# Performance work log

Measured on AMD Instinct MI355X. Metric: run time of the kernel, lower is better.

Reference implementation:

```python
import jax, jax.numpy as jnp
import numpy as np

B, S, E, H = 8, 1024, 512, 8
NEG = -1e10


def setup_inputs() -> dict:
    key = jax.random.key(0)
    ks = jax.random.split(key, 8)
    k = jax.random.normal(ks[0], (B, S, E), dtype=jnp.float32)
    v = jax.random.normal(ks[1], (B, S, E), dtype=jnp.float32)
    q = jax.random.normal(ks[2], (B, S, E), dtype=jnp.float32)
    # causal mask, broadcastable like torch masked_fill
    mask = jnp.tril(jnp.ones((S, S), dtype=jnp.int32))[None, None]
    sc = 1.0 / np.sqrt(E)
    Wk = jax.random.normal(ks[3], (H * E, E), dtype=jnp.float32) * sc
    Wq = jax.random.normal(ks[4], (H * E, E), dtype=jnp.float32) * sc
    Wv = jax.random.normal(ks[5], (H * E, E), dtype=jnp.float32) * sc
    Wo = jax.random.normal(ks[6], (E, H * E), dtype=jnp.float32) * (1.0 / np.sqrt(H * E))
    bo = jnp.zeros((E,), dtype=jnp.float32)
    return {"k": k, "v": v, "q": q, "mask": mask,
            "Wk": Wk, "Wq": Wq, "Wv": Wv, "Wo": Wo, "bo": bo}


def reference(k, v, q, mask, Wk, Wq, Wv, Wo, bo):
    b, q_len, e = q.shape
    k_len, v_len = k.shape[1], v.shape[1]
    h = Wk.shape[0] // e
    scale = jnp.sqrt(jnp.asarray(e // h, dtype=jnp.float32))
    # projections E -> H*E (torch Linear: x @ W.T)
    wk = (k @ Wk.T).reshape(b, h, k_len, e)   # raw reshape, matches torch .view
    wq = (q @ Wq.T).reshape(b, h, q_len, e)
    wv = (v @ Wv.T).reshape(b, h, v_len, e)
    energy = jnp.einsum('bhqe,bhke->bhqk', wq, wk)
    energy = jnp.where(mask == 0, NEG, energy)  # mask applied BEFORE scaling, as in source
    energy = energy / scale
    attn = jax.nn.softmax(energy, axis=-1)
    f = jnp.einsum('bhqk,bhke->bhqe', attn, wv)
    f = jnp.transpose(f, (0, 2, 1, 3)).reshape(b, q_len, h * e)
    return f @ Wo.T + bo
```

## Files before the change

kernel.cpp:

```cpp
#include <hip/hip_runtime.h>


typedef _Float16 half8 __attribute__((ext_vector_type(8)));
typedef _Float16 half4v __attribute__((ext_vector_type(4)));
typedef float f32x4 __attribute__((ext_vector_type(4)));

typedef __attribute__((address_space(3))) unsigned int lds_u32_t;
typedef __attribute__((address_space(1))) unsigned int g_u32_t;

__device__ __forceinline__ void glds16(const void* g, void* l) {
  __builtin_amdgcn_global_load_lds((const g_u32_t*)g, (lds_u32_t*)l, 16, 0, 0);
}

__device__ __forceinline__ void stage_panel64(const _Float16* __restrict__ G,
                                              int ld, _Float16* Ls, int tid) {
  int w = tid >> 6;
#pragma unroll
  for (int e = 0; e < 4; e++) {
    int X = e * 8192 + tid * 16;
    int r = X >> 7;
    int s = (X >> 4) & 7;
    glds16(G + (size_t)r * ld + (((s ^ (r & 7)) & 7) << 3),
           Ls + ((e * 8192 + w * 1024) >> 1));
  }
}

template <int NT>
__device__ __forceinline__ void gemm256_core(const _Float16* __restrict__ A,
                                             const _Float16* __restrict__ B,
                                             int lda, int ldb,
                                             _Float16* smem, f32x4 (&acc)[8][4]) {
  int tid = (int)threadIdx.x;
  int w = tid >> 6, lane = tid & 63;
  int wr = (w >> 2) * 128, wc = (w & 3) * 64;
  int lr = lane & 15, hi = lane >> 4, l7 = lane & 7;

  stage_panel64(A, lda, smem, tid);
  stage_panel64(B, ldb, smem + 16384, tid);

  for (int t = 0; t < NT; t++) {
    asm volatile("s_waitcnt vmcnt(0)" ::: "memory");
    __builtin_amdgcn_s_barrier();
    __builtin_amdgcn_sched_barrier(0);
    if (t + 1 < NT) {
      _Float16* nb = smem + ((t + 1) & 1) * 32768;
      stage_panel64(A + (t + 1) * 64, lda, nb, tid);
      stage_panel64(B + (t + 1) * 64, ldb, nb + 16384, tid);
    }
    const _Float16* As = smem + (t & 1) * 32768;
    const _Float16* Bs = As + 16384;
    half8 a[4], b[4];
#pragma unroll
    for (int ks = 0; ks < 2; ks++) {
      int seg = (((ks * 4 + hi) ^ l7) & 7) << 3;
#pragma unroll
      for (int ni = 0; ni < 4; ni++)
        b[ni] = *(const half8*)&Bs[(wc + ni * 16 + lr) * 64 + seg];
#pragma unroll
      for (int mi = 0; mi < 4; mi++)
        a[mi] = *(const half8*)&As[(wr + mi * 16 + lr) * 64 + seg];
      __builtin_amdgcn_sched_barrier(0);
      __builtin_amdgcn_s_barrier();
      asm volatile("s_waitcnt lgkmcnt(0)" ::: "memory");
      __builtin_amdgcn_sched_barrier(0);
      __builtin_amdgcn_s_setprio(1);
#pragma unroll
      for (int mi = 0; mi < 4; mi++)
#pragma unroll
        for (int ni = 0; ni < 4; ni++)
          acc[mi][ni] = __builtin_amdgcn_mfma_f32_16x16x32_f16(a[mi], b[ni],
                                                               acc[mi][ni], 0, 0, 0);
      __builtin_amdgcn_s_setprio(0);
      __builtin_amdgcn_sched_barrier(0);
#pragma unroll
      for (int mi = 0; mi < 4; mi++)
        a[mi] = *(const half8*)&As[(wr + (mi + 4) * 16 + lr) * 64 + seg];
      __builtin_amdgcn_sched_barrier(0);
      __builtin_amdgcn_s_barrier();
      asm volatile("s_waitcnt lgkmcnt(0)" ::: "memory");
      __builtin_amdgcn_sched_barrier(0);
      __builtin_amdgcn_s_setprio(1);
#pragma unroll
      for (int mi = 0; mi < 4; mi++)
#pragma unroll
        for (int ni = 0; ni < 4; ni++)
          acc[mi + 4][ni] = __builtin_amdgcn_mfma_f32_16x16x32_f16(a[mi], b[ni],
                                                                   acc[mi + 4][ni], 0, 0, 0);
      __builtin_amdgcn_s_setprio(0);
      __builtin_amdgcn_sched_barrier(0);
    }
  }
  __syncthreads();
}

__device__ __forceinline__ void epilogue256(f32x4 (&acc)[8][4], _Float16* lds,
                                            _Float16* Cp, size_t cOff,
                                            int i0, int j0, int ldc) {
  int tid = (int)threadIdx.x;
  int w = tid >> 6, lane = tid & 63;
  int wr = (w >> 2) * 128, wc = (w & 3) * 64;
  int r0 = (lane >> 4) * 4, cl = lane & 15;
  _Float16* T = lds + w * 8192;
#pragma unroll
  for (int mi = 0; mi < 8; mi++)
#pragma unroll
    for (int ni = 0; ni < 4; ni++) {
      int colb = ni * 16 + cl;
#pragma unroll
      for (int r = 0; r < 4; r++) {
        int row = mi * 16 + r0 + r;
        T[row * 64 + ((((colb >> 3) ^ row) & 7) << 3) + (colb & 7)] =
            (_Float16)acc[mi][ni][r];
      }
    }
#pragma unroll
  for (int st = 0; st < 16; st++) {
    int row = st * 8 + (lane >> 3);
    int c8 = lane & 7;
    half8 h = *(const half8*)&T[row * 64 + (((c8 ^ row) & 7) << 3)];
    *(half8*)(Cp + cOff + (size_t)(i0 + wr + row) * ldc + j0 + wc + c8 * 8) = h;
  }
}

template <int HG>
__global__ __launch_bounds__(512, 2) void proj256(const _Float16* __restrict__ in16,
                                                  const _Float16* __restrict__ W16,
                                                  _Float16* __restrict__ Qp,
                                                  _Float16* __restrict__ Kp,
                                                  _Float16* __restrict__ Vp) {
  __shared__ __align__(16) _Float16 smem[65536];
  int x = (int)blockIdx.x, Y = (int)blockIdx.y;
  int it = x >> 4, jt = x & 15;
  const _Float16* A = in16 + (size_t)Y * HG * 524288 + (size_t)it * 131072;
  const _Float16* B = W16 + (size_t)Y * 2097152 + (size_t)jt * 131072;
  _Float16* C = (Y == 0 ? Qp : (Y == 1 ? Kp : Vp));
  f32x4 acc[8][4] = {};
  gemm256_core<8>(A, B, 512, 512, smem, acc);
  epilogue256(acc, smem, C, 0, it * 256, jt * 256, 4096);
}

template <int HG>
__global__ __launch_bounds__(512, 2) void vwo256(const _Float16* __restrict__ Vp,
                                                 const _Float16* __restrict__ WoG,
                                                 _Float16* __restrict__ VWo) {
  __shared__ __align__(16) _Float16 smem[65536];
  int x = (int)blockIdx.x, Y = (int)blockIdx.y, Z = (int)blockIdx.z;
  size_t z = (size_t)Z * HG + Y;
  int i0 = (x >> 2) * 256, j0 = (x & 3) * 256;
  const _Float16* A = WoG + (size_t)Y * 512 + (size_t)i0 * 4096;
  const _Float16* B = Vp + z * 524288 + (size_t)j0 * 512;
  f32x4 acc[8][4] = {};
  gemm256_core<8>(A, B, 4096, 512, smem, acc);
  epilogue256(acc, smem, VWo, z * 524288, i0, j0, 1024);
}

template <int HG>
__global__ __launch_bounds__(512, 2) void energy256(const _Float16* __restrict__ Qp,
                                                    const _Float16* __restrict__ Kp,
                                                    _Float16* __restrict__ E) {
  __shared__ __align__(16) _Float16 smem[65536];
  int x = (int)blockIdx.x, Y = (int)blockIdx.y, Z = (int)blockIdx.z;
  size_t z = (size_t)Z * HG + Y;
  int ti = (int)((sqrtf(8.0f * x + 1.0f) - 1.0f) * 0.5f);
  if (ti * (ti + 1) / 2 > x) ti--;
  else if ((ti + 1) * (ti + 2) / 2 <= x) ti++;
  int tj = x - ti * (ti + 1) / 2;
  int i0 = ti * 256, j0 = tj * 256;
  const _Float16* A = Qp + z * 524288 + (size_t)i0 * 512;
  const _Float16* B = Kp + z * 524288 + (size_t)j0 * 512;
  f32x4 acc[8][4] = {};
  gemm256_core<8>(A, B, 512, 512, smem, acc);
  epilogue256(acc, smem, E, z * 1048576, i0, j0, 1024);
}

template <int HL>
__device__ __forceinline__ void gemm_core(const _Float16* A, const _Float16* B,
                                          int lda, int ldb, int kmax,
                                          long sAh, long sBh,
                                          _Float16* As, _Float16* Bs,
                                          f32x4 (&acc)[4][4]) {
  int tid = (int)threadIdx.x;
  int w = tid >> 6, lane = tid & 63;
  int wr = (w >> 1) * 64, wc = (w & 1) * 64;
  int lr = lane & 15, lk = (lane >> 4) * 8;
  int srow = lane >> 2, sseg = (lane & 3) * 8;

  for (int h = 0; h < HL; h++) {
    const _Float16* Ah = A + (size_t)h * sAh;
    const _Float16* Bh = B + (size_t)h * sBh;
    for (int k0 = 0; k0 < kmax; k0 += 64) {
      __syncthreads();
#pragma unroll
      for (int p = 0; p < 2; p++)
#pragma unroll
        for (int t = 0; t < 2; t++) {
          glds16(Ah + (size_t)(w * 32 + t * 16 + srow) * lda + k0 + p * 32 + sseg,
                 As + p * 4096 + (w * 32 + t * 16) * 32);
          glds16(Bh + (size_t)(w * 32 + t * 16 + srow) * ldb + k0 + p * 32 + sseg,
                 Bs + p * 4096 + (w * 32 + t * 16) * 32);
        }
      __syncthreads();
#pragma unroll
      for (int p = 0; p < 2; p++) {
        half8 a[4], b[4];
#pragma unroll
        for (int mi = 0; mi < 4; mi++)
          a[mi] = *(half8*)&As[p * 4096 + (wr + mi * 16 + lr) * 32 + lk];
#pragma unroll
        for (int ni = 0; ni < 4; ni++)
          b[ni] = *(half8*)&Bs[p * 4096 + (wc + ni * 16 + lr) * 32 + lk];
#pragma unroll
        for (int mi = 0; mi < 4; mi++)
#pragma unroll
          for (int ni = 0; ni < 4; ni++)
            acc[mi][ni] =
                __builtin_amdgcn_mfma_f32_16x16x32_f16(a[mi], b[ni], acc[mi][ni], 0, 0, 0);
      }
    }
  }
}

__device__ __forceinline__ void epilogue_atomic(f32x4 (&acc)[4][4], float* Cp,
                                                size_t cOff, int i0, int j0, int ldc) {
  int tid = (int)threadIdx.x;
  int w = tid >> 6, lane = tid & 63;
  int wr = (w >> 1) * 64, wc = (w & 1) * 64;
  int r0 = (lane >> 4) * 4, col = lane & 15;
#pragma unroll
  for (int mi = 0; mi < 4; mi++)
#pragma unroll
    for (int ni = 0; ni < 4; ni++)
#pragma unroll
      for (int r = 0; r < 4; r++)
        unsafeAtomicAdd(Cp + cOff + (size_t)(i0 + wr + mi * 16 + r0 + r) * ldc +
                            j0 + wc + ni * 16 + col,
                        acc[mi][ni][r]);
}

template <int HG, int HL>
__global__ __launch_bounds__(256) void pv_kernel(const _Float16* __restrict__ E,
                                                 const _Float16* __restrict__ VWo,
                                                 float* __restrict__ out) {
  __shared__ __align__(16) _Float16 smem[17408];
  int x = (int)blockIdx.x, Y = (int)blockIdx.y, Z = (int)blockIdx.z;
  int i0 = (x >> 2) * 128, j0 = (x & 3) * 128;
  int kmax = i0 + 128;
  const _Float16* A = E + ((size_t)Z * HG + (size_t)Y * HL) * 1048576 + (size_t)i0 * 1024;
  const _Float16* B = VWo + ((size_t)Z * HG + (size_t)Y * HL) * 524288 + (size_t)j0 * 1024;
  f32x4 acc[4][4] = {};
  gemm_core<HL>(A, B, 1024, 1024, kmax, 1048576, 524288, smem, smem + 8192, acc);
  epilogue_atomic(acc, out, (size_t)Z * 524288, i0, j0, 512);
}

__global__ __launch_bounds__(256) void softmax_rows(void* __restrict__ Ep) {
  int R = (int)blockIdx.x * 4 + ((int)threadIdx.x >> 6);
  int lane = (int)threadIdx.x & 63;
  int i = R & 1023;
  int nt = (i >> 8) + 1;
  _Float16* row = (_Float16*)Ep + (size_t)R * 1024;
  float x[16];
  float m = -3.0e38f;
#pragma unroll
  for (int t = 0; t < 4; t++) {
    if (t < nt) {
      int j0 = t * 256 + lane * 4;
      half4v h = *(const half4v*)(row + j0);
#pragma unroll
      for (int c = 0; c < 4; c++) {
        float v = (j0 + c <= i) ? (float)h[c] * 0.125f : -3.0e38f;
        x[t * 4 + c] = v;
        m = fmaxf(m, v);
      }
    }
  }
#pragma unroll
  for (int s = 32; s > 0; s >>= 1) m = fmaxf(m, __shfl_xor(m, s, 64));
  float p[16];
  float sum = 0.0f;
#pragma unroll
  for (int t = 0; t < 4; t++) {
    if (t < nt) {
#pragma unroll
      for (int c = 0; c < 4; c++) {
        p[t * 4 + c] = exp2f((x[t * 4 + c] - m) * 1.44269504f);
        sum += p[t * 4 + c];
      }
    }
  }
#pragma unroll
  for (int s = 32; s > 0; s >>= 1) sum += __shfl_xor(sum, s, 64);
  float inv = 1.0f / sum;
#pragma unroll
  for (int t = 0; t < 4; t++) {
    if (t < nt) {
      int j0 = t * 256 + lane * 4;
      half4v h;
#pragma unroll
      for (int c = 0; c < 4; c++) h[c] = (_Float16)(p[t * 4 + c] * inv);
      *(half4v*)(row + j0) = h;
    }
  }
}

__global__ __launch_bounds__(256) void wbconv(const float* __restrict__ Wq,
                                              const float* __restrict__ Wk,
                                              const float* __restrict__ Wv,
                                              const float* __restrict__ Wo,
                                              _Float16* __restrict__ W16,
                                              float* __restrict__ out,
                                              const float* __restrict__ bo) {
  int bx = (int)blockIdx.x;
  if (bx < 4096) {
    size_t base = ((size_t)bx * 256 + threadIdx.x) * 8;
    int wid = (int)(base >> 21);
    size_t off = base & 2097151;
    const float* src = wid == 0 ? Wq : (wid == 1 ? Wk : (wid == 2 ? Wv : Wo));
    float4 a = *(const float4*)(src + off);
    float4 b = *(const float4*)(src + off + 4);
    half8 h;
    h[0] = (_Float16)a.x; h[1] = (_Float16)a.y; h[2] = (_Float16)a.z; h[3] = (_Float16)a.w;
    h[4] = (_Float16)b.x; h[5] = (_Float16)b.y; h[6] = (_Float16)b.z; h[7] = (_Float16)b.w;
    *(half8*)(W16 + base) = h;
  } else {
    size_t idx = ((size_t)(bx - 4096) * 256 + threadIdx.x) * 4;
    *(float4*)(out + idx) = *(const float4*)(bo + (idx & 511));
  }
}

template <int HG>
__global__ __launch_bounds__(256) void inconv(const float* __restrict__ q,
                                              const float* __restrict__ k,
                                              const float* __restrict__ v,
                                              _Float16* __restrict__ dst) {
  int Y = (int)blockIdx.y;
  size_t base = ((size_t)blockIdx.x * 256 + threadIdx.x) * 8;
  size_t b = base / (HG * 65536);
  size_t within = base - b * (HG * 65536);
  const float* src = (Y == 0 ? q : (Y == 1 ? k : v)) + b * 524288 + within;
  float4 a = ((const float4*)src)[0];
  float4 c = ((const float4*)src)[1];
  half8 h;
  h[0] = (_Float16)a.x; h[1] = (_Float16)a.y; h[2] = (_Float16)a.z; h[3] = (_Float16)a.w;
  h[4] = (_Float16)c.x; h[5] = (_Float16)c.y; h[6] = (_Float16)c.z; h[7] = (_Float16)c.w;
  *(half8*)(dst + (size_t)Y * HG * 524288 + base) = h;
}

template <int HG>
static void run_pipeline(const float* q_in, const float* k_in, const float* v_in,
                         const float* Wq, const float* Wk, const float* Wv,
                         const float* Wo, const float* bo, float* out, char* ws,
                         hipStream_t stream) {
  const int NG = 8 / HG;
  const long zc = 8 * HG;
  _Float16* W16 = (_Float16*)ws;
  _Float16* in16 = W16 + 8388608;
  _Float16* Qp = in16 + 3L * HG * 524288;
  _Float16* Kp = Qp + zc * 524288;
  _Float16* VWo = Kp + zc * 524288;
  _Float16* E = VWo + zc * 524288;
  _Float16* Vp = E;
  _Float16* Wo16 = W16 + 3 * 2097152;
  dim3 blk(256);
  dim3 blk5(512);

  wbconv<<<dim3(8192), blk, 0, stream>>>(Wq, Wk, Wv, Wo, W16, out, bo);

  constexpr int HL = (HG >= 2) ? 2 : 1;
  constexpr int YS = HG / HL;

  for (int g = 0; g < NG; g++) {
    inconv<HG><<<dim3(HG * 256, 3), blk, 0, stream>>>(
        q_in + (size_t)g * HG * 65536, k_in + (size_t)g * HG * 65536,
        v_in + (size_t)g * HG * 65536, in16);

    proj256<HG><<<dim3(HG * 64, 3), blk5, 0, stream>>>(in16, W16, Qp, Kp, Vp);

    vwo256<HG><<<dim3(8, HG, 8), blk5, 0, stream>>>(
        Vp, Wo16 + (size_t)g * HG * 512, VWo);

    energy256<HG><<<dim3(10, HG, 8), blk5, 0, stream>>>(Qp, Kp, E);

    softmax_rows<<<dim3(zc * 256), blk, 0, stream>>>(E);

    pv_kernel<HG, HL><<<dim3(32, YS, 8), blk, 0, stream>>>(E, VWo, out);
  }
}

extern "C" void kernel_launch(void* const* d_in, const int* in_sizes, int n_in,
                              void* d_out, int out_size, void* d_ws, size_t ws_size,
                              hipStream_t stream) {
  const float* k_in = (const float*)d_in[0];
  const float* v_in = (const float*)d_in[1];
  const float* q_in = (const float*)d_in[2];
  const float* Wk = (const float*)d_in[4];
  const float* Wq = (const float*)d_in[5];
  const float* Wv = (const float*)d_in[6];
  const float* Wo = (const float*)d_in[7];
  const float* bo = (const float*)d_in[8];
  float* out = (float*)d_out;
  char* ws = (char*)d_ws;

  if (ws_size >= (size_t)197132288)
    run_pipeline<4>(q_in, k_in, v_in, Wq, Wk, Wv, Wo, bo, out, ws, stream);
  else if (ws_size >= (size_t)106954752)
    run_pipeline<2>(q_in, k_in, v_in, Wq, Wk, Wv, Wo, bo, out, ws, stream);
  else
    run_pipeline<1>(q_in, k_in, v_in, Wq, Wk, Wv, Wo, bo, out, ws, stream);
}
```

Measured before the change: 530.1 us.

## Halve GEMM K-panel to 32 with paired-row LDS layout and smaller shared memory

Reworks the 256x256 GEMM core to stage K-panels of 32 instead of 64, using a paired-row swizzled LDS layout so each half8 read covers two rows. It doubles the iteration count and halves LDS use from 128KB to 64KB per block. The epilogue is split into two halves so it fits in the smaller buffer. The aim is to raise occupancy or LDS headroom and cut per-iteration load latency, at the cost of more barriers per unit of K.

```diff
diff --git a/kernel.cpp b/kernel.cpp
--- a/kernel.cpp
+++ b/kernel.cpp
@@ -10,19 +10,6 @@
 
 __device__ __forceinline__ void glds16(const void* g, void* l) {
   __builtin_amdgcn_global_load_lds((const g_u32_t*)g, (lds_u32_t*)l, 16, 0, 0);
-}
-
-__device__ __forceinline__ void stage_panel64(const _Float16* __restrict__ G,
-                                              int ld, _Float16* Ls, int tid) {
-  int w = tid >> 6;
-#pragma unroll
-  for (int e = 0; e < 4; e++) {
-    int X = e * 8192 + tid * 16;
-    int r = X >> 7;
-    int s = (X >> 4) & 7;
-    glds16(G + (size_t)r * ld + (((s ^ (r & 7)) & 7) << 3),
-           Ls + ((e * 8192 + w * 1024) >> 1));
-  }
 }
 
 template <int NT>
@@ -32,63 +19,81 @@
                                              _Float16* smem, f32x4 (&acc)[8][4]) {
   int tid = (int)threadIdx.x;
   int w = tid >> 6, lane = tid & 63;
-  int wr = (w >> 2) * 128, wc = (w & 3) * 64;
-  int lr = lane & 15, hi = lane >> 4, l7 = lane & 7;
-
-  stage_panel64(A, lda, smem, tid);
-  stage_panel64(B, ldb, smem + 16384, tid);
-
+  int wr2 = (w >> 2) * 64;
+  int wc2 = (w & 3) * 32;
+  int lr = lane & 15, hi = lane >> 4;
+  int sp = ((((lane & 1) << 2) + hi) ^ ((lr >> 1) & 7)) << 3;
+  int aBase = (wr2 + (lr >> 1)) * 64 + sp;
+  int bBase = 8192 + (wc2 + (lr >> 1)) * 64 + sp;
+
+  int srcA[2], srcB[2], dstE[2];
+#pragma unroll
+  for (int e = 0; e < 2; e++) {
+    int X = e * 8192 + tid * 16;
+    int rp = X >> 7;
+    int s = ((X >> 4) & 7) ^ (rp & 7);
+    int g = 2 * rp + (s >> 2);
+    int c = s & 3;
+    srcA[e] = g * lda + (c << 3);
+    srcB[e] = g * ldb + (c << 3);
+    dstE[e] = e * 4096 + w * 512;
+  }
+
+#pragma unroll
+  for (int e = 0; e < 2; e++) {
+    glds16(A + srcA[e], smem + dstE[e]);
+    glds16(B + srcB[e], smem + 8192 + dstE[e]);
+  }
+
+#pragma unroll
   for (int t = 0; t < NT; t++) {
-    asm volatile("s_waitcnt vmcnt(0)" ::: "memory");
+    __syncthreads();
+    const _Float16* As = smem + (t & 1) * 16384;
+    half8 a[4], b[4];
+#pragma unroll
+    for (int ni = 0; ni < 4; ni++)
+      b[ni] = *(const half8*)&As[bBase + ni * 512];
+#pragma unroll
+    for (int mi = 0; mi < 4; mi++)
+      a[mi] = *(const half8*)&As[aBase + mi * 512];
+    if (t + 1 < NT) {
+      _Float16* nb = smem + ((t + 1) & 1) * 16384;
+#pragma unroll
+      for (int e = 0; e < 2; e++) {
+        glds16(A + srcA[e] + (t + 1) * 32, nb + dstE[e]);
+        glds16(B + srcB[e] + (t + 1) * 32, nb + 8192 + dstE[e]);
+      }
+    }
+    __builtin_amdgcn_sched_barrier(0);
     __builtin_amdgcn_s_barrier();
-    __builtin_amdgcn_sched_barrier(0);
-    if (t + 1 < NT) {
-      _Float16* nb = smem + ((t + 1) & 1) * 32768;
-      stage_panel64(A + (t + 1) * 64, lda, nb, tid);
-      stage_panel64(B + (t + 1) * 64, ldb, nb + 16384, tid);
-    }
-    const _Float16* As = smem + (t & 1) * 32768;
-    const _Float16* Bs = As + 16384;
-    half8 a[4], b[4];
-#pragma unroll
-    for (int ks = 0; ks < 2; ks++) {
-      int seg = (((ks * 4 + hi) ^ l7) & 7) << 3;
+    asm volatile("s_waitcnt lgkmcnt(0)" ::: "memory");
+    __builtin_amdgcn_sched_barrier(0);
+    __builtin_amdgcn_s_setprio(1);
+#pragma unroll
+    for (int mi = 0; mi < 4; mi++)
 #pragma unroll
       for (int ni = 0; ni < 4; ni++)
-        b[ni] = *(const half8*)&Bs[(wc + ni * 16 + lr) * 64 + seg];
-#pragma unroll
-      for (int mi = 0; mi < 4; mi++)
-        a[mi] = *(const half8*)&As[(wr + mi * 16 + lr) * 64 + seg];
-      __builtin_amdgcn_sched_barrier(0);
-      __builtin_amdgcn_s_barrier();
-      asm volatile("s_waitcnt lgkmcnt(0)" ::: "memory");
-      __builtin_amdgcn_sched_barrier(0);
-      __builtin_amdgcn_s_setprio(1);
-#pragma unroll
-      for (int mi = 0; mi < 4; mi++)
-#pragma unroll
-        for (int ni = 0; ni < 4; ni++)
-          acc[mi][ni] = __builtin_amdgcn_mfma_f32_16x16x32_f16(a[mi], b[ni],
-                                                               acc[mi][ni], 0, 0, 0);
-      __builtin_amdgcn_s_setprio(0);
-      __builtin_amdgcn_sched_barrier(0);
-#pragma unroll
-      for (int mi = 0; mi < 4; mi++)
-        a[mi] = *(const half8*)&As[(wr + (mi + 4) * 16 + lr) * 64 + seg];
-      __builtin_amdgcn_sched_barrier(0);
-      __builtin_amdgcn_s_barrier();
-      asm volatile("s_waitcnt lgkmcnt(0)" ::: "memory");
-      __builtin_amdgcn_sched_barrier(0);
-      __builtin_amdgcn_s_setprio(1);
-#pragma unroll
-      for (int mi = 0; mi < 4; mi++)
-#pragma unroll
-        for (int ni = 0; ni < 4; ni++)
-          acc[mi + 4][ni] = __builtin_amdgcn_mfma_f32_16x16x32_f16(a[mi], b[ni],
-                                                                   acc[mi + 4][ni], 0, 0, 0);
-      __builtin_amdgcn_s_setprio(0);
-      __builtin_amdgcn_sched_barrier(0);
-    }
+        acc[mi][ni] = __builtin_amdgcn_mfma_f32_16x16x32_f16(a[mi], b[ni],
+                                                             acc[mi][ni], 0, 0, 0);
+    __builtin_amdgcn_s_setprio(0);
+    __builtin_amdgcn_sched_barrier(0);
+    __builtin_amdgcn_s_barrier();
+#pragma unroll
+    for (int mi = 0; mi < 4; mi++)
+      a[mi] = *(const half8*)&As[aBase + (mi + 4) * 512];
+    __builtin_amdgcn_sched_barrier(0);
+    __builtin_amdgcn_s_barrier();
+    asm volatile("s_waitcnt lgkmcnt(0)" ::: "memory");
+    __builtin_amdgcn_sched_barrier(0);
+    __builtin_amdgcn_s_setprio(1);
+#pragma unroll
+    for (int mi = 0; mi < 4; mi++)
+#pragma unroll
+      for (int ni = 0; ni < 4; ni++)
+        acc[mi + 4][ni] = __builtin_amdgcn_mfma_f32_16x16x32_f16(a[mi], b[ni],
+                                                                 acc[mi + 4][ni], 0, 0, 0);
+    __builtin_amdgcn_s_setprio(0);
+    __builtin_amdgcn_sched_barrier(0);
   }
   __syncthreads();
 }
@@ -100,25 +105,28 @@
   int w = tid >> 6, lane = tid & 63;
   int wr = (w >> 2) * 128, wc = (w & 3) * 64;
   int r0 = (lane >> 4) * 4, cl = lane & 15;
-  _Float16* T = lds + w * 8192;
-#pragma unroll
-  for (int mi = 0; mi < 8; mi++)
-#pragma unroll
-    for (int ni = 0; ni < 4; ni++) {
-      int colb = ni * 16 + cl;
-#pragma unroll
-      for (int r = 0; r < 4; r++) {
-        int row = mi * 16 + r0 + r;
-        T[row * 64 + ((((colb >> 3) ^ row) & 7) << 3) + (colb & 7)] =
-            (_Float16)acc[mi][ni][r];
+  _Float16* T = lds + w * 4096;
+#pragma unroll
+  for (int h = 0; h < 2; h++) {
+#pragma unroll
+    for (int mi = 0; mi < 4; mi++)
+#pragma unroll
+      for (int ni = 0; ni < 4; ni++) {
+        int colb = ni * 16 + cl;
+#pragma unroll
+        for (int r = 0; r < 4; r++) {
+          int row = mi * 16 + r0 + r;
+          T[row * 64 + ((((colb >> 3) ^ row) & 7) << 3) + (colb & 7)] =
+              (_Float16)acc[h * 4 + mi][ni][r];
+        }
       }
-    }
-#pragma unroll
-  for (int st = 0; st < 16; st++) {
-    int row = st * 8 + (lane >> 3);
-    int c8 = lane & 7;
-    half8 h = *(const half8*)&T[row * 64 + (((c8 ^ row) & 7) << 3)];
-    *(half8*)(Cp + cOff + (size_t)(i0 + wr + row) * ldc + j0 + wc + c8 * 8) = h;
+#pragma unroll
+    for (int st = 0; st < 8; st++) {
+      int row = st * 8 + (lane >> 3);
+      int c8 = lane & 7;
+      half8 hh = *(const half8*)&T[row * 64 + (((c8 ^ row) & 7) << 3)];
+      *(half8*)(Cp + cOff + (size_t)(i0 + wr + h * 64 + row) * ldc + j0 + wc + c8 * 8) = hh;
+    }
   }
 }
 
@@ -128,14 +136,14 @@
                                                   _Float16* __restrict__ Qp,
                                                   _Float16* __restrict__ Kp,
                                                   _Float16* __restrict__ Vp) {
-  __shared__ __align__(16) _Float16 smem[65536];
+  __shared__ __align__(16) _Float16 smem[32768];
   int x = (int)blockIdx.x, Y = (int)blockIdx.y;
   int it = x >> 4, jt = x & 15;
   const _Float16* A = in16 + (size_t)Y * HG * 524288 + (size_t)it * 131072;
   const _Float16* B = W16 + (size_t)Y * 2097152 + (size_t)jt * 131072;
   _Float16* C = (Y == 0 ? Qp : (Y == 1 ? Kp : Vp));
   f32x4 acc[8][4] = {};
-  gemm256_core<8>(A, B, 512, 512, smem, acc);
+  gemm256_core<16>(A, B, 512, 512, smem, acc);
   epilogue256(acc, smem, C, 0, it * 256, jt * 256, 4096);
 }
 
@@ -143,14 +151,14 @@
 __global__ __launch_bounds__(512, 2) void vwo256(const _Float16* __restrict__ Vp,
                                                  const _Float16* __restrict__ WoG,
                                                  _Float16* __restrict__ VWo) {
-  __shared__ __align__(16) _Float16 smem[65536];
+  __shared__ __align__(16) _Float16 smem[32768];
   int x = (int)blockIdx.x, Y = (int)blockIdx.y, Z = (int)blockIdx.z;
   size_t z = (size_t)Z * HG + Y;
   int i0 = (x >> 2) * 256, j0 = (x & 3) * 256;
   const _Float16* A = WoG + (size_t)Y * 512 + (size_t)i0 * 4096;
   const _Float16* B = Vp + z * 524288 + (size_t)j0 * 512;
   f32x4 acc[8][4] = {};
-  gemm256_core<8>(A, B, 4096, 512, smem, acc);
+  gemm256_core<16>(A, B, 4096, 512, smem, acc);
   epilogue256(acc, smem, VWo, z * 524288, i0, j0, 1024);
 }
 
@@ -158,7 +166,7 @@
 __global__ __launch_bounds__(512, 2) void energy256(const _Float16* __restrict__ Qp,
                                                     const _Float16* __restrict__ Kp,
                                                     _Float16* __restrict__ E) {
-  __shared__ __align__(16) _Float16 smem[65536];
+  __shared__ __align__(16) _Float16 smem[32768];
   int x = (int)blockIdx.x, Y = (int)blockIdx.y, Z = (int)blockIdx.z;
   size_t z = (size_t)Z * HG + Y;
   int ti = (int)((sqrtf(8.0f * x + 1.0f) - 1.0f) * 0.5f);
@@ -169,7 +177,7 @@
   const _Float16* A = Qp + z * 524288 + (size_t)i0 * 512;
   const _Float16* B = Kp + z * 524288 + (size_t)j0 * 512;
   f32x4 acc[8][4] = {};
-  gemm256_core<8>(A, B, 512, 512, smem, acc);
+  gemm256_core<16>(A, B, 512, 512, smem, acc);
   epilogue256(acc, smem, E, z * 1048576, i0, j0, 1024);
 }
 
```

After: 535.7 us. No clear change (+1.1%).
